# Kernel tuning notes

Hardware: AMD Instinct MI355X
Metric: run time of the kernel (lower is better)

## Reference

```python
import jax, jax.numpy as jnp
import numpy as np

B, C, H, W = 8, 256, 64, 64
IC = 128  # inter_channels = C // reduction


def setup_inputs() -> dict:
    key = jax.random.key(0)
    ks = jax.random.split(key, 9)
    s_in = 1.0 / np.sqrt(C)
    s_ic = 1.0 / np.sqrt(IC)
    return {
        "x": jax.random.normal(ks[0], (B, C, H, W), jnp.float32),
        "wg": jax.random.normal(ks[1], (IC, C), jnp.float32) * s_in,
        "bg": jax.random.normal(ks[2], (IC,), jnp.float32) * s_in,
        "wt": jax.random.normal(ks[3], (IC, C), jnp.float32) * s_in,
        "bt": jax.random.normal(ks[4], (IC,), jnp.float32) * s_in,
        "wp": jax.random.normal(ks[5], (IC, C), jnp.float32) * s_in,
        "bp": jax.random.normal(ks[6], (IC,), jnp.float32) * s_in,
        "wm": jax.random.normal(ks[7], (C, IC), jnp.float32) * s_ic,
        "bm": jax.random.normal(ks[8], (C,), jnp.float32) * s_ic,
    }


def reference(x, wg, bg, wt, bt, wp, bp, wm, bm):
    b, c, h, w = x.shape
    n = h * w
    xf = x.reshape(b, c, n)  # [B, C, N]
    # 1x1 convs are channel matmuls; relu applied after each (as in source)
    g = jax.nn.relu(jnp.einsum('ic,bcn->bni', wg, xf) + bg)          # [B, N, IC]
    theta = jax.nn.relu(jnp.einsum('ic,bcn->bni', wt, xf) + bt)      # [B, N, IC]
    phi = jax.nn.relu(jnp.einsum('ic,bcn->bin', wp, xf) + bp[:, None])  # [B, IC, N]
    scores = jnp.einsum('bni,bim->bnm', theta, phi)                  # [B, N, N] (no scaling)
    attn = jax.nn.softmax(scores, axis=-1)
    out = jnp.einsum('bnm,bmi->bni', attn, g)                        # [B, N, IC]
    mask = jax.nn.relu(jnp.einsum('oc,bnc->bon', wm, out) + bm[None, :, None])
    return mask.reshape(b, c, h, w) + x
```

## Files before the change

### kernel.cpp

```cpp
#include <hip/hip_runtime.h>

typedef __bf16 bf16x8 __attribute__((ext_vector_type(8)));
typedef float f32x4 __attribute__((ext_vector_type(4)));
typedef float f32x16 __attribute__((ext_vector_type(16)));
typedef unsigned short ushort8 __attribute__((ext_vector_type(8)));
typedef unsigned short ushort4v __attribute__((ext_vector_type(4)));
typedef unsigned int uint4v __attribute__((ext_vector_type(4)));

union Frag {
  ushort8 u;
  bf16x8 b;
  uint4v w;
};

__device__ __forceinline__ unsigned short f2bf(float f) {
  unsigned int u = __float_as_uint(f);
  u += 0x7fffu + ((u >> 16) & 1u);
  return (unsigned short)(u >> 16);
}

__device__ __forceinline__ f32x4 fz4() {
  f32x4 v; v[0] = 0.f; v[1] = 0.f; v[2] = 0.f; v[3] = 0.f; return v;
}

__device__ __forceinline__ f32x16 fz16() {
  f32x16 v;
#pragma unroll
  for (int i = 0; i < 16; ++i) v[i] = 0.f;
  return v;
}

#define MFMA16(a, b, c) __builtin_amdgcn_mfma_f32_16x16x32_bf16(a, b, c, 0, 0, 0)
#define MFMA32(a, b, c) __builtin_amdgcn_mfma_f32_32x32x16_bf16(a, b, c, 0, 0, 0)

#define LOG2E 1.4426950408889634f


__global__ void k_prep(const float* __restrict__ wg, const float* __restrict__ wt,
                       const float* __restrict__ wp, const float* __restrict__ wm,
                       unsigned short* __restrict__ wcat, unsigned short* __restrict__ wmb) {
  int t = blockIdx.x * 256 + threadIdx.x;
  if (t < 98304) {
    int o = t >> 8;
    const float* src = (o < 128) ? wt : ((o < 256) ? wp : wg);
    wcat[t] = f2bf(src[(o & 127) * 256 + (t & 255)]);
  }
  if (t < 32768) wmb[t] = f2bf(wm[t]);
}

__device__ __forceinline__ void stage_x(const float* __restrict__ x, int bx, int pt0,
                                        unsigned short* xb, int tid) {
  int c0 = (tid >> 2) * 4;
  int psub = (tid & 3) * 16;
  const float* xbase = x + (size_t)bx * 256 * 4096 + pt0;
  for (int ppc = 0; ppc < 4; ++ppc) {
    int p0 = psub + ppc * 4;
    f32x4 r0 = *(const f32x4*)(xbase + (size_t)(c0 + 0) * 4096 + p0);
    f32x4 r1 = *(const f32x4*)(xbase + (size_t)(c0 + 1) * 4096 + p0);
    f32x4 r2 = *(const f32x4*)(xbase + (size_t)(c0 + 2) * 4096 + p0);
    f32x4 r3 = *(const f32x4*)(xbase + (size_t)(c0 + 3) * 4096 + p0);
    for (int e = 0; e < 4; ++e) {
      ushort4v wv;
      wv[0] = f2bf(r0[e]); wv[1] = f2bf(r1[e]); wv[2] = f2bf(r2[e]); wv[3] = f2bf(r3[e]);
      *(ushort4v*)&xb[(p0 + e) * 264 + c0] = wv;
    }
  }
}

__global__ __launch_bounds__(256, 2) void k_proj(
    const float* __restrict__ x, const unsigned short* __restrict__ wcat,
    const float* __restrict__ bt, const float* __restrict__ bp,
    const float* __restrict__ bg,
    unsigned short* __restrict__ theta, unsigned short* __restrict__ phiS,
    unsigned short* __restrict__ vS) {
  __shared__ unsigned short xb[64 * 264];
  int gb = blockIdx.x >> 6;
  size_t ob_off = (size_t)gb * 524288;
  int pt0 = (blockIdx.x & 63) << 6;
  int tid = threadIdx.x;
  stage_x(x, gb, pt0, xb, tid);
  __syncthreads();
  int l = tid & 63, w = tid >> 6, lr = l & 15, lg = l >> 4;
  int obase = w * 64;
  f32x4 acc[4][4];
  f32x4 accg[8];
  for (int i = 0; i < 4; ++i) for (int j = 0; j < 4; ++j) acc[i][j] = fz4();
  for (int i = 0; i < 8; ++i) accg[i] = fz4();
  for (int kc = 0; kc < 8; ++kc) {
    int ko = kc * 32 + 8 * lg;
    Frag wa[4], xq[4];
    for (int ot = 0; ot < 4; ++ot)
      wa[ot].u = *(const ushort8*)(wcat + (size_t)(obase + ot * 16 + lr) * 256 + ko);
    for (int pt = 0; pt < 4; ++pt)
      xq[pt].u = *(const ushort8*)&xb[(pt * 16 + lr) * 264 + ko];
    for (int ot = 0; ot < 4; ++ot)
      for (int pt = 0; pt < 4; ++pt)
        acc[ot][pt] = MFMA16(wa[ot].b, xq[pt].b, acc[ot][pt]);
    for (int ot = 0; ot < 8; ++ot) {
      Frag wb;
      wb.u = *(const ushort8*)(wcat + (size_t)(256 + ot * 16 + lr) * 256 + ko);
      accg[ot] = MFMA16(xq[w].b, wb.b, accg[ot]);
    }
  }
  for (int ot = 0; ot < 4; ++ot) {
    int o0 = obase + ot * 16 + 4 * lg;
    float bias[4];
    for (int j = 0; j < 4; ++j) bias[j] = (o0 < 128) ? bt[o0 + j] : bp[o0 + j - 128];
    for (int pt = 0; pt < 4; ++pt) {
      int n = pt0 + pt * 16 + lr;
      ushort4v wv;
      if (o0 < 128) {
        for (int j = 0; j < 4; ++j) {
          float v = acc[ot][pt][j] + bias[j];
          wv[j] = f2bf(v > 0.f ? v * LOG2E : 0.f);
        }
        *(ushort4v*)(theta + ob_off + (size_t)n * 128 + o0) = wv;
      } else {
        for (int j = 0; j < 4; ++j) {
          float v = acc[ot][pt][j] + bias[j];
          wv[j] = f2bf(v > 0.f ? v : 0.f);
        }
        int oc = o0 - 128;
        size_t a = (size_t)(n >> 5) * 4096 + (size_t)(oc >> 4) * 512 +
                   (size_t)((oc >> 3) & 1) * 256 + (size_t)(n & 31) * 8 + (oc & 7);
        *(ushort4v*)(phiS + ob_off + a) = wv;
      }
    }
  }
  for (int ot = 0; ot < 8; ++ot) {
    int o = ot * 16 + lr;
    float bias = bg[o];
    int n0 = pt0 + w * 16 + 4 * lg;
    ushort4v wv;
    for (int j = 0; j < 4; ++j) {
      float v = accg[ot][j] + bias;
      wv[j] = f2bf(v > 0.f ? v : 0.f);
    }
    size_t a = (size_t)(n0 >> 5) * 4096 +
               (size_t)((o >> 5) * 2 + ((n0 >> 4) & 1)) * 512 +
               (size_t)((((n0 >> 3) & 1) << 5) | (o & 31)) * 8 + (n0 & 7);
    *(ushort4v*)(vS + ob_off + a) = wv;
  }
}

__global__ __launch_bounds__(256, 3) void k_attn(
    const unsigned short* __restrict__ theta, const unsigned short* __restrict__ phiS,
    const unsigned short* __restrict__ vS, unsigned short* __restrict__ out_nm) {
  __shared__ float osum[32][132];
  __shared__ float mls[4][32][2];
  int bid = blockIdx.x;
  int b = bid & 7;
  int q0 = (bid >> 3) << 5;
  int tid = threadIdx.x;
  int l = tid & 63, wid = tid >> 6;
  int ml = l & 31, hi = l >> 5;
  int l8 = l * 8;

  const size_t tbase = ((size_t)b << 12) * 128;
  const unsigned short* pS = phiS + (size_t)b * 524288;
  const unsigned short* vSb = vS + (size_t)b * 524288;

  Frag qf[8];
#pragma unroll
  for (int kc = 0; kc < 8; ++kc)
    qf[kc].u = *(const ushort8*)(theta + tbase +
        (size_t)(q0 + ml) * 128 + kc * 16 + 8 * hi);

  f32x16 oacc[4];
#pragma unroll
  for (int db = 0; db < 4; ++db) oacc[db] = fz16();
  float m = -1e30f, sden = 0.f;

  int t0 = wid * 32;

  for (int kt = 0; kt < 32; ++kt) {
    int t = t0 + kt;

    Frag pa[8];
#pragma unroll
    for (int kc = 0; kc < 8; ++kc)
      pa[kc].u = *(const ushort8*)(pS + (size_t)t * 4096 + kc * 512 + l8);

    f32x16 sacc = fz16();
#pragma unroll
    for (int kc = 0; kc < 8; ++kc) sacc = MFMA32(pa[kc].b, qf[kc].b, sacc);

    Frag vt[8];
#pragma unroll
    for (int t8 = 0; t8 < 8; ++t8)
      vt[t8].u = *(const ushort8*)(vSb + (size_t)t * 4096 + t8 * 512 + l8);

    float m8[8];
#pragma unroll
    for (int j = 0; j < 8; ++j) m8[j] = fmaxf(sacc[j], sacc[j + 8]);
    float t1 = fmaxf(fmaxf(m8[0], m8[1]), m8[2]);
    float t2 = fmaxf(fmaxf(m8[3], m8[4]), m8[5]);
    float t3 = fmaxf(m8[6], m8[7]);
    float mt = fmaxf(fmaxf(t1, t2), t3);
    mt = fmaxf(mt, __shfl_xor(mt, 32));
    if (!__all(mt <= m + 24.0f)) {
      float mn = fmaxf(m, mt);
      float sc = __builtin_exp2f(m - mn);
      sden *= sc;
#pragma unroll
      for (int db = 0; db < 4; ++db) oacc[db] *= sc;
      m = mn;
    }
    float p[16];
#pragma unroll
    for (int r = 0; r < 16; ++r) p[r] = __builtin_exp2f(sacc[r] - m);
    float s8[8];
#pragma unroll
    for (int j = 0; j < 8; ++j) s8[j] = p[j] + p[j + 8];
    float ps = ((s8[0] + s8[1]) + (s8[2] + s8[3])) + ((s8[4] + s8[5]) + (s8[6] + s8[7]));
    ps += __shfl_xor(ps, 32);
    sden += ps;

    unsigned wpk[8], pw[8];
#pragma unroll
    for (int j = 0; j < 8; ++j) {
      unsigned u0 = __float_as_uint(p[2 * j]);
      unsigned u1 = __float_as_uint(p[2 * j + 1]);
      wpk[j] = (u1 & 0xFFFF0000u) | (u0 >> 16);
    }
#pragma unroll
    for (int j = 0; j < 8; ++j) pw[j] = (unsigned)__shfl_xor((int)wpk[j], 32);
    Frag bf0, bf1;
    bf0.w[0] = hi ? pw[2] : wpk[0];
    bf0.w[1] = hi ? pw[3] : wpk[1];
    bf0.w[2] = hi ? wpk[2] : pw[0];
    bf0.w[3] = hi ? wpk[3] : pw[1];
    bf1.w[0] = hi ? pw[6] : wpk[4];
    bf1.w[1] = hi ? pw[7] : wpk[5];
    bf1.w[2] = hi ? wpk[6] : pw[4];
    bf1.w[3] = hi ? wpk[7] : pw[5];

#pragma unroll
    for (int db = 0; db < 4; ++db) {
      oacc[db] = MFMA32(vt[db * 2].b, bf0.b, oacc[db]);
      oacc[db] = MFMA32(vt[db * 2 + 1].b, bf1.b, oacc[db]);
    }
  }

  if (l < 32) { mls[wid][l][0] = m; mls[wid][l][1] = sden; }
  __syncthreads();
  float M = fmaxf(fmaxf(mls[0][ml][0], mls[1][ml][0]),
                  fmaxf(mls[2][ml][0], mls[3][ml][0]));
  float sc = __builtin_exp2f(m - M);
  for (int w = 0; w < 4; ++w) {
    if (wid == w) {
#pragma unroll
      for (int db = 0; db < 4; ++db)
#pragma unroll
        for (int r = 0; r < 16; ++r) {
          int d = db * 32 + (r & 3) + 8 * (r >> 2) + 4 * hi;
          if (w == 0) osum[ml][d] = oacc[db][r] * sc;
          else        osum[ml][d] += oacc[db][r] * sc;
        }
    }
    __syncthreads();
  }
  {
    int row = wid * 8 + (l >> 3);
    int d0 = (l & 7) * 16;
    float Mx = fmaxf(fmaxf(mls[0][row][0], mls[1][row][0]),
                     fmaxf(mls[2][row][0], mls[3][row][0]));
    float Lt = 0.f;
    for (int w = 0; w < 4; ++w) Lt += mls[w][row][1] * __builtin_exp2f(mls[w][row][0] - Mx);
    float inv = 1.0f / Lt;
    ushort8 w1;
    for (int k = 0; k < 8; ++k) w1[k] = f2bf(osum[row][d0 + k] * inv);
    ushort8 w2;
    for (int k = 0; k < 8; ++k) w2[k] = f2bf(osum[row][d0 + 8 + k] * inv);
    size_t a = (size_t)b * 524288 + (size_t)(q0 >> 5) * 4096 +
               (size_t)(d0 >> 4) * 512 + (size_t)row * 8;
    *(ushort8*)(out_nm + a) = w1;
    *(ushort8*)(out_nm + a + 256) = w2;
  }
}

__global__ __launch_bounds__(256, 2) void k_mask(
    const unsigned short* __restrict__ wmb, const unsigned short* __restrict__ out_nm,
    const float* __restrict__ bm, const float* __restrict__ x,
    float* __restrict__ out) {
  int gb = blockIdx.x >> 6;
  size_t boff = (size_t)gb * 524288;
  int n0 = (blockIdx.x & 63) << 6;
  int tid = threadIdx.x;
  int l = tid & 63, w = tid >> 6, lr = l & 15, lg = l >> 4;
  int ob = w * 64;
  f32x4 acc[4][4];
  for (int i = 0; i < 4; ++i) for (int j = 0; j < 4; ++j) acc[i][j] = fz4();
  for (int kc = 0; kc < 4; ++kc) {
    int ko = kc * 32 + 8 * lg;
    int kc2 = kc * 2 + (lg >> 1), hi2 = lg & 1;
    Frag wa[4], xq[4];
    for (int ot = 0; ot < 4; ++ot)
      wa[ot].u = *(const ushort8*)(wmb + (size_t)(ob + ot * 16 + lr) * 128 + ko);
    for (int nt = 0; nt < 4; ++nt) {
      int t = (n0 >> 5) + (nt >> 1);
      int mln = ((nt & 1) << 4) + lr;
      xq[nt].u = *(const ushort8*)(out_nm + boff + (size_t)t * 4096 +
                                   (size_t)kc2 * 512 + (size_t)(hi2 * 32 + mln) * 8);
    }
    for (int ot = 0; ot < 4; ++ot)
      for (int nt = 0; nt < 4; ++nt)
        acc[ot][nt] = MFMA16(wa[ot].b, xq[nt].b, acc[ot][nt]);
  }
  for (int ot = 0; ot < 4; ++ot) {
    int o0 = ob + ot * 16 + 4 * lg;
    for (int nt = 0; nt < 4; ++nt) {
      int n = n0 + nt * 16 + lr;
      for (int j = 0; j < 4; ++j) {
        size_t idx = ((size_t)(gb << 8) + o0 + j) * 4096 + n;
        float v = acc[ot][nt][j] + bm[o0 + j];
        v = v > 0.f ? v : 0.f;
        out[idx] = v + x[idx];
      }
    }
  }
}

extern "C" void kernel_launch(void* const* d_in, const int* in_sizes, int n_in,
                              void* d_out, int out_size, void* d_ws, size_t ws_size,
                              hipStream_t stream) {
  const float* x  = (const float*)d_in[0];
  const float* wg = (const float*)d_in[1];
  const float* bg = (const float*)d_in[2];
  const float* wt = (const float*)d_in[3];
  const float* bt = (const float*)d_in[4];
  const float* wp = (const float*)d_in[5];
  const float* bp = (const float*)d_in[6];
  const float* wm = (const float*)d_in[7];
  const float* bm = (const float*)d_in[8];
  float* out = (float*)d_out;

  const size_t SLAB = 524288;
  unsigned short* wcat  = (unsigned short*)d_ws;
  unsigned short* wmb   = wcat + 98304;
  unsigned short* theta = wmb + 32768;
  unsigned short* phiS  = theta + 8 * SLAB;
  unsigned short* vS    = phiS + 8 * SLAB;

  k_prep<<<384, 256, 0, stream>>>(wg, wt, wp, wm, wcat, wmb);
  k_proj<<<512, 256, 0, stream>>>(x, wcat, bt, bp, bg, theta, phiS, vS);
  k_attn<<<1024, 256, 0, stream>>>(theta, phiS, vS, theta );
  k_mask<<<512, 256, 0, stream>>>(wmb, theta, bm, x, out);
}
```

Before: 169.3 us.

## Retile attention to 64 queries per block with 2x2 wave split and phi prefetch

Each attention block now covers 64 queries instead of 32. Its four waves split into two query halves and two key halves, so each wave walks 64 key tiles instead of 32 and the cross-wave softmax merge only spans two partials. This halves the phi/V reads per query and the number of blocks. The phi fragments for the next key tile are loaded before the current softmax step, so the loads overlap with compute. The costs are lower launch occupancy (launch bounds go from 3 to 2 blocks per SM), a larger LDS buffer, and a final prefetch that reads just past the batch slab.

```diff
diff --git a/kernel.cpp b/kernel.cpp
--- a/kernel.cpp
+++ b/kernel.cpp
@@ -143,18 +143,20 @@
   }
 }
 
-__global__ __launch_bounds__(256, 3) void k_attn(
+__global__ __launch_bounds__(256, 2) void k_attn(
     const unsigned short* __restrict__ theta, const unsigned short* __restrict__ phiS,
     const unsigned short* __restrict__ vS, unsigned short* __restrict__ out_nm) {
-  __shared__ float osum[32][132];
+  __shared__ float osum[64][132];
   __shared__ float mls[4][32][2];
   int bid = blockIdx.x;
   int b = bid & 7;
-  int q0 = (bid >> 3) << 5;
+  int bq0 = (bid >> 3) << 6;
   int tid = threadIdx.x;
   int l = tid & 63, wid = tid >> 6;
   int ml = l & 31, hi = l >> 5;
   int l8 = l * 8;
+  int qh = wid & 1, kh = wid >> 1;
+  int q0 = bq0 + qh * 32;
 
   const size_t tbase = ((size_t)b << 12) * 128;
   const unsigned short* pS = phiS + (size_t)b * 524288;
@@ -171,15 +173,15 @@
   for (int db = 0; db < 4; ++db) oacc[db] = fz16();
   float m = -1e30f, sden = 0.f;
 
-  int t0 = wid * 32;
-
-  for (int kt = 0; kt < 32; ++kt) {
+  int t0 = kh * 64;
+
+  Frag pa[8];
+#pragma unroll
+  for (int kc = 0; kc < 8; ++kc)
+    pa[kc].u = *(const ushort8*)(pS + (size_t)t0 * 4096 + kc * 512 + l8);
+
+  for (int kt = 0; kt < 64; ++kt) {
     int t = t0 + kt;
-
-    Frag pa[8];
-#pragma unroll
-    for (int kc = 0; kc < 8; ++kc)
-      pa[kc].u = *(const ushort8*)(pS + (size_t)t * 4096 + kc * 512 + l8);
 
     f32x16 sacc = fz16();
 #pragma unroll
@@ -189,6 +191,10 @@
 #pragma unroll
     for (int t8 = 0; t8 < 8; ++t8)
       vt[t8].u = *(const ushort8*)(vSb + (size_t)t * 4096 + t8 * 512 + l8);
+
+#pragma unroll
+    for (int kc = 0; kc < 8; ++kc)
+      pa[kc].u = *(const ushort8*)(pS + (size_t)(t + 1) * 4096 + kc * 512 + l8);
 
     float m8[8];
 #pragma unroll
@@ -244,38 +250,51 @@
 
   if (l < 32) { mls[wid][l][0] = m; mls[wid][l][1] = sden; }
   __syncthreads();
-  float M = fmaxf(fmaxf(mls[0][ml][0], mls[1][ml][0]),
-                  fmaxf(mls[2][ml][0], mls[3][ml][0]));
-  float sc = __builtin_exp2f(m - M);
-  for (int w = 0; w < 4; ++w) {
-    if (wid == w) {
+  {
+    float M = fmaxf(mls[qh][ml][0], mls[qh + 2][ml][0]);
+    float sc = __builtin_exp2f(m - M);
+    int orow = qh * 32 + ml;
+    if (kh == 0) {
 #pragma unroll
       for (int db = 0; db < 4; ++db)
 #pragma unroll
         for (int r = 0; r < 16; ++r) {
           int d = db * 32 + (r & 3) + 8 * (r >> 2) + 4 * hi;
-          if (w == 0) osum[ml][d] = oacc[db][r] * sc;
-          else        osum[ml][d] += oacc[db][r] * sc;
+          osum[orow][d] = oacc[db][r] * sc;
         }
     }
     __syncthreads();
+    if (kh == 1) {
+#pragma unroll
+      for (int db = 0; db < 4; ++db)
+#pragma unroll
+        for (int r = 0; r < 16; ++r) {
+          int d = db * 32 + (r & 3) + 8 * (r >> 2) + 4 * hi;
+          osum[orow][d] += oacc[db][r] * sc;
+        }
+    }
+    __syncthreads();
   }
   {
-    int row = wid * 8 + (l >> 3);
-    int d0 = (l & 7) * 16;
-    float Mx = fmaxf(fmaxf(mls[0][row][0], mls[1][row][0]),
-                     fmaxf(mls[2][row][0], mls[3][row][0]));
-    float Lt = 0.f;
-    for (int w = 0; w < 4; ++w) Lt += mls[w][row][1] * __builtin_exp2f(mls[w][row][0] - Mx);
+    int row = tid & 63;
+    int mlr = row & 31, qhr = row >> 5;
+    int t_ = (bq0 + row) >> 5;
+    float Mx = fmaxf(mls[qhr][mlr][0], mls[qhr + 2][mlr][0]);
+    float Lt = mls[qhr][mlr][1] * __builtin_exp2f(mls[qhr][mlr][0] - Mx) +
+               mls[qhr + 2][mlr][1] * __builtin_exp2f(mls[qhr + 2][mlr][0] - Mx);
     float inv = 1.0f / Lt;
-    ushort8 w1;
-    for (int k = 0; k < 8; ++k) w1[k] = f2bf(osum[row][d0 + k] * inv);
-    ushort8 w2;
-    for (int k = 0; k < 8; ++k) w2[k] = f2bf(osum[row][d0 + 8 + k] * inv);
-    size_t a = (size_t)b * 524288 + (size_t)(q0 >> 5) * 4096 +
-               (size_t)(d0 >> 4) * 512 + (size_t)row * 8;
-    *(ushort8*)(out_nm + a) = w1;
-    *(ushort8*)(out_nm + a + 256) = w2;
+#pragma unroll
+    for (int u = 0; u < 2; ++u) {
+      int d0 = (wid + 4 * u) * 16;
+      ushort8 w1;
+      for (int k = 0; k < 8; ++k) w1[k] = f2bf(osum[row][d0 + k] * inv);
+      ushort8 w2;
+      for (int k = 0; k < 8; ++k) w2[k] = f2bf(osum[row][d0 + 8 + k] * inv);
+      size_t a = (size_t)b * 524288 + (size_t)t_ * 4096 +
+                 (size_t)(d0 >> 4) * 512 + (size_t)mlr * 8;
+      *(ushort8*)(out_nm + a) = w1;
+      *(ushort8*)(out_nm + a + 256) = w2;
+    }
   }
 }
 
@@ -344,6 +363,6 @@
 
   k_prep<<<384, 256, 0, stream>>>(wg, wt, wp, wm, wcat, wmb);
   k_proj<<<512, 256, 0, stream>>>(x, wcat, bt, bp, bg, theta, phiS, vS);
-  k_attn<<<1024, 256, 0, stream>>>(theta, phiS, vS, theta );
+  k_attn<<<512, 256, 0, stream>>>(theta, phiS, vS, theta );
   k_mask<<<512, 256, 0, stream>>>(wmb, theta, bm, x, out);
 }
```

Result: faster. 163.5 us (-3.4%).
